# Kernel tuning notes

Hardware: AMD Instinct MI355X
Metric: run time of the kernel (lower is better)

The kernel has to match this reference:

```python
import jax, jax.numpy as jnp
import numpy as np

BETA = 0.95      # LIF leak
LR = 2e-06       # Hebbian learning rate
THRESH = 1.0     # snntorch Leaky default threshold, reset-by-subtraction
NUM_INPUTS = 8192
NUM_HIDDEN = 8192


def surrogate(x):
    # 1 / (pi * (1 + (pi*x)^2))
    return 1.0 / (jnp.pi * (1.0 + (jnp.pi * x) ** 2))


def setup_inputs() -> dict:
    key = jax.random.key(0)
    ks = jax.random.split(key, 8)
    I, H = NUM_INPUTS, NUM_HIDDEN
    inp = jax.random.normal(ks[0], (I,), jnp.float32)
    bf = jnp.float32(1.0)
    fc_w = jax.random.normal(ks[1], (H, I), jnp.float32) / np.float32(np.sqrt(I))
    fc_b = jnp.zeros((H,), jnp.float32)
    pred_w = jax.random.normal(ks[2], (H, H), jnp.float32) / np.float32(np.sqrt(H))
    retro_w = jax.random.normal(ks[3], (H, H), jnp.float32) / np.float32(np.sqrt(H))
    feedback = jax.random.normal(ks[4], (H,), jnp.float32) * 0.1
    mem = jax.random.uniform(ks[5], (H,), jnp.float32)
    cur_prev = jax.random.normal(ks[6], (H,), jnp.float32)
    prev_inp = jax.random.normal(ks[7], (I,), jnp.float32)
    return {"inp": inp, "bf": bf, "fc_w": fc_w, "fc_b": fc_b,
            "pred_w": pred_w, "retro_w": retro_w, "feedback": feedback,
            "mem": mem, "cur_prev": cur_prev, "prev_inp": prev_inp}


def reference(inp, bf, fc_w, fc_b, pred_w, retro_w, feedback, mem, cur_prev, prev_inp):
    # ---- LIF step (snntorch Leaky, reset by subtraction) ----
    cur = fc_w @ inp + fc_b                       # [H]
    mem_new = BETA * mem + cur                    # [H]
    spk = (mem_new > THRESH).astype(cur.dtype)    # [H]
    mem_out = mem_new - spk * THRESH              # [H]

    # ---- Hebbian / CLAPP weight updates (training branch) ----
    retrodiction = retro_w @ spk                  # [H]
    dW_pred = (LR * bf) * jnp.outer(feedback, spk)        # [H,H]
    pred_w_new = pred_w + dW_pred
    retro_w_new = retro_w + dW_pred.T

    # diag(v) @ outer(a, b) == outer(v * a, b): avoid materializing [H,H] diag
    dW = (LR * bf) * jnp.outer(feedback * surrogate(cur), inp)       # [H,I]
    dW = dW + bf * jnp.outer(retrodiction * surrogate(cur_prev), prev_inp)
    fc_w_new = fc_w + dW

    feedback_new = pred_w_new @ spk               # [H]
    return spk, mem_out, fc_w_new, pred_w_new, retro_w_new, feedback_new
```

## Files before the change

kernel.cpp:

```cpp
#include <hip/hip_runtime.h>
#include <math.h>

static constexpr int HN = 8192;
static constexpr int IN = 8192;
static constexpr float LRF = 2.0e-6f;

__device__ __forceinline__ float surrogate_f(float x) {
    const float PI = 3.14159265358979323846f;
    float px = PI * x;
    return 1.0f / (PI * fmaf(px, px, 1.0f));
}

__device__ __forceinline__ float block_reduce_f32(float v) {
#pragma unroll
    for (int off = 32; off > 0; off >>= 1) v += __shfl_down(v, off);
    __shared__ float s[4];
    if ((threadIdx.x & 63) == 0) s[threadIdx.x >> 6] = v;
    __syncthreads();
    return s[0] + s[1] + s[2] + s[3];
}

__global__ __launch_bounds__(256) void k_lif(
    const float* __restrict__ fc_w, const float* __restrict__ inp,
    const float* __restrict__ fc_b, const float* __restrict__ mem,
    float* __restrict__ out_spk, float* __restrict__ out_mem,
    float* __restrict__ ws_cur, float* __restrict__ ws_spk)
{
    const int row = blockIdx.x;
    const int t = threadIdx.x;
    const float4* __restrict__ wr = (const float4*)(fc_w + (size_t)row * IN);
    const float4* __restrict__ ip = (const float4*)inp;
    double acc = 0.0;
#pragma unroll
    for (int j = 0; j < IN / 4 / 256; ++j) {
        float4 w = wr[t + j * 256];
        float4 x = ip[t + j * 256];
        acc += (double)w.x * (double)x.x;
        acc += (double)w.y * (double)x.y;
        acc += (double)w.z * (double)x.z;
        acc += (double)w.w * (double)x.w;
    }
#pragma unroll
    for (int off = 32; off > 0; off >>= 1) acc += __shfl_down(acc, off);
    __shared__ double sacc[4];
    if ((t & 63) == 0) sacc[t >> 6] = acc;
    __syncthreads();
    if (t == 0) {
        double c = sacc[0] + sacc[1] + sacc[2] + sacc[3] + (double)fc_b[row];
        double m = 0.95 * (double)mem[row] + c;
        float spk = (m > 1.0) ? 1.0f : 0.0f;
        out_spk[row] = spk;
        ws_spk[row]  = spk;
        out_mem[row] = (float)(m - (double)spk);
        ws_cur[row]  = (float)c;
    }
}

__global__ __launch_bounds__(256) void k_bc(
    const float* __restrict__ retro_w, const float* __restrict__ pred_w,
    const float* __restrict__ feedback, const float* __restrict__ bfp,
    const float* __restrict__ ws_spk,
    float* __restrict__ out_pred, float* __restrict__ out_retro,
    float* __restrict__ out_fb, float* __restrict__ ws_ret)
{
    const float lrbf = LRF * bfp[0];
    const int t = threadIdx.x;
    const float4* __restrict__ spk4 = (const float4*)ws_spk;
    if (blockIdx.x < HN) {
        const int row = blockIdx.x;
        const float4* __restrict__ wr = (const float4*)(retro_w + (size_t)row * HN);
        float4* __restrict__ orow = (float4*)(out_retro + (size_t)row * HN);
        const float4* __restrict__ fb4 = (const float4*)feedback;
        const float coef = lrbf * ws_spk[row];
        float acc = 0.0f;
#pragma unroll
        for (int j = 0; j < HN / 4 / 256; ++j) {
            int idx = t + j * 256;
            float4 w = wr[idx];
            float4 s = spk4[idx];
            float4 f = fb4[idx];
            acc += w.x * s.x + w.y * s.y + w.z * s.z + w.w * s.w;
            float4 o;
            o.x = w.x + coef * f.x;
            o.y = w.y + coef * f.y;
            o.z = w.z + coef * f.z;
            o.w = w.w + coef * f.w;
            orow[idx] = o;
        }
        float r = block_reduce_f32(acc);
        if (t == 0) ws_ret[row] = r;
    } else {
        const int row = blockIdx.x - HN;
        const float4* __restrict__ wr = (const float4*)(pred_w + (size_t)row * HN);
        float4* __restrict__ orow = (float4*)(out_pred + (size_t)row * HN);
        const float coef = lrbf * feedback[row];
        float acc = 0.0f;
#pragma unroll
        for (int j = 0; j < HN / 4 / 256; ++j) {
            int idx = t + j * 256;
            float4 w = wr[idx];
            float4 s = spk4[idx];
            float4 o;
            o.x = w.x + coef * s.x;
            o.y = w.y + coef * s.y;
            o.z = w.z + coef * s.z;
            o.w = w.w + coef * s.w;
            orow[idx] = o;
            acc += o.x * s.x + o.y * s.y + o.z * s.z + o.w * s.w;
        }
        float r = block_reduce_f32(acc);
        if (t == 0) out_fb[row] = r;
    }
}

__global__ __launch_bounds__(256) void k_fc(
    const float* __restrict__ fc_w, const float* __restrict__ inp,
    const float* __restrict__ prev_inp, const float* __restrict__ feedback,
    const float* __restrict__ cur_prev, const float* __restrict__ bfp,
    const float* __restrict__ ws_cur, const float* __restrict__ ws_ret,
    float* __restrict__ out_fcw)
{
    const float bf = bfp[0];
    const int row = blockIdx.x;
    const int t = threadIdx.x;
    const float a = LRF * bf * feedback[row] * surrogate_f(ws_cur[row]);
    const float b = bf * ws_ret[row] * surrogate_f(cur_prev[row]);
    const float4* __restrict__ wr = (const float4*)(fc_w + (size_t)row * IN);
    const float4* __restrict__ ip = (const float4*)inp;
    const float4* __restrict__ pp = (const float4*)prev_inp;
    float4* __restrict__ orow = (float4*)(out_fcw + (size_t)row * IN);
#pragma unroll
    for (int j = 0; j < IN / 4 / 256; ++j) {
        int idx = t + j * 256;
        float4 w = wr[idx];
        float4 x = ip[idx];
        float4 p = pp[idx];
        float4 o;
        o.x = w.x + a * x.x + b * p.x;
        o.y = w.y + a * x.y + b * p.y;
        o.z = w.z + a * x.z + b * p.z;
        o.w = w.w + a * x.w + b * p.w;
        orow[idx] = o;
    }
}

extern "C" void kernel_launch(void* const* d_in, const int* in_sizes, int n_in,
                              void* d_out, int out_size, void* d_ws, size_t ws_size,
                              hipStream_t stream)
{
    const float* inp      = (const float*)d_in[0];
    const float* bf       = (const float*)d_in[1];
    const float* fc_w     = (const float*)d_in[2];
    const float* fc_b     = (const float*)d_in[3];
    const float* pred_w   = (const float*)d_in[4];
    const float* retro_w  = (const float*)d_in[5];
    const float* feedback = (const float*)d_in[6];
    const float* mem      = (const float*)d_in[7];
    const float* cur_prev = (const float*)d_in[8];
    const float* prev_inp = (const float*)d_in[9];

    float* out = (float*)d_out;
    float* out_spk   = out;
    float* out_mem   = out + HN;
    float* out_fcw   = out + 2 * HN;
    float* out_pred  = out_fcw + (size_t)HN * IN;
    float* out_retro = out_pred + (size_t)HN * HN;
    float* out_fb    = out_retro + (size_t)HN * HN;

    float* ws = (float*)d_ws;
    float* ws_cur = ws;
    float* ws_spk = ws + HN;
    float* ws_ret = ws + 2 * HN;

    k_lif<<<HN, 256, 0, stream>>>(fc_w, inp, fc_b, mem, out_spk, out_mem, ws_cur, ws_spk);
    k_bc<<<2 * HN, 256, 0, stream>>>(retro_w, pred_w, feedback, bf, ws_spk,
                                     out_pred, out_retro, out_fb, ws_ret);
    k_fc<<<HN, 256, 0, stream>>>(fc_w, inp, prev_inp, feedback, cur_prev, bf,
                                 ws_cur, ws_ret, out_fcw);
}
```

Before: 359.1 us.

## Fuse fc_w update into retro block and use nontemporal loads/stores

Merges the fc_w update kernel into the retro_w block, so each retro row computes its retrodiction and then updates the matching fc_w row directly. This drops one launch and the workspace round trip for the retrodiction values. Nontemporal loads and stores are applied to the large weight streams to reduce cache pollution. Block work becomes unbalanced: retro blocks now do two row passes while pred blocks do one, which could lengthen the tail.

```diff
diff --git a/kernel.cpp b/kernel.cpp
--- a/kernel.cpp
+++ b/kernel.cpp
@@ -4,6 +4,8 @@
 static constexpr int HN = 8192;
 static constexpr int IN = 8192;
 static constexpr float LRF = 2.0e-6f;
+
+typedef float f32x4 __attribute__((ext_vector_type(4)));
 
 __device__ __forceinline__ float surrogate_f(float x) {
     const float PI = 3.14159265358979323846f;
@@ -28,13 +30,13 @@
 {
     const int row = blockIdx.x;
     const int t = threadIdx.x;
-    const float4* __restrict__ wr = (const float4*)(fc_w + (size_t)row * IN);
-    const float4* __restrict__ ip = (const float4*)inp;
+    const f32x4* __restrict__ wr = (const f32x4*)(fc_w + (size_t)row * IN);
+    const f32x4* __restrict__ ip = (const f32x4*)inp;
     double acc = 0.0;
 #pragma unroll
     for (int j = 0; j < IN / 4 / 256; ++j) {
-        float4 w = wr[t + j * 256];
-        float4 x = ip[t + j * 256];
+        f32x4 w = wr[t + j * 256];
+        f32x4 x = ip[t + j * 256];
         acc += (double)w.x * (double)x.x;
         acc += (double)w.y * (double)x.y;
         acc += (double)w.z * (double)x.z;
@@ -56,91 +58,83 @@
     }
 }
 
-__global__ __launch_bounds__(256) void k_bc(
+__global__ __launch_bounds__(256) void k_fused(
     const float* __restrict__ retro_w, const float* __restrict__ pred_w,
+    const float* __restrict__ fc_w, const float* __restrict__ inp,
+    const float* __restrict__ prev_inp,
     const float* __restrict__ feedback, const float* __restrict__ bfp,
-    const float* __restrict__ ws_spk,
+    const float* __restrict__ cur_prev,
+    const float* __restrict__ ws_spk, const float* __restrict__ ws_cur,
     float* __restrict__ out_pred, float* __restrict__ out_retro,
-    float* __restrict__ out_fb, float* __restrict__ ws_ret)
+    float* __restrict__ out_fcw, float* __restrict__ out_fb)
 {
-    const float lrbf = LRF * bfp[0];
+    const float bf = bfp[0];
+    const float lrbf = LRF * bf;
     const int t = threadIdx.x;
-    const float4* __restrict__ spk4 = (const float4*)ws_spk;
+    const f32x4* __restrict__ spk4 = (const f32x4*)ws_spk;
+
     if (blockIdx.x < HN) {
         const int row = blockIdx.x;
-        const float4* __restrict__ wr = (const float4*)(retro_w + (size_t)row * HN);
-        float4* __restrict__ orow = (float4*)(out_retro + (size_t)row * HN);
-        const float4* __restrict__ fb4 = (const float4*)feedback;
+        const f32x4* __restrict__ wr = (const f32x4*)(retro_w + (size_t)row * HN);
+        f32x4* __restrict__ orow = (f32x4*)(out_retro + (size_t)row * HN);
+        const f32x4* __restrict__ fb4 = (const f32x4*)feedback;
         const float coef = lrbf * ws_spk[row];
         float acc = 0.0f;
 #pragma unroll
         for (int j = 0; j < HN / 4 / 256; ++j) {
             int idx = t + j * 256;
-            float4 w = wr[idx];
-            float4 s = spk4[idx];
-            float4 f = fb4[idx];
+            f32x4 w = __builtin_nontemporal_load(&wr[idx]);
+            f32x4 s = spk4[idx];
+            f32x4 f = fb4[idx];
             acc += w.x * s.x + w.y * s.y + w.z * s.z + w.w * s.w;
-            float4 o;
+            f32x4 o;
             o.x = w.x + coef * f.x;
             o.y = w.y + coef * f.y;
             o.z = w.z + coef * f.z;
             o.w = w.w + coef * f.w;
-            orow[idx] = o;
+            __builtin_nontemporal_store(o, &orow[idx]);
         }
-        float r = block_reduce_f32(acc);
-        if (t == 0) ws_ret[row] = r;
+        float retrod = block_reduce_f32(acc);
+        const float a = lrbf * feedback[row] * surrogate_f(ws_cur[row]);
+        const float b = bf * retrod * surrogate_f(cur_prev[row]);
+        const f32x4* __restrict__ fwr = (const f32x4*)(fc_w + (size_t)row * IN);
+        const f32x4* __restrict__ ip = (const f32x4*)inp;
+        const f32x4* __restrict__ pp = (const f32x4*)prev_inp;
+        f32x4* __restrict__ forow = (f32x4*)(out_fcw + (size_t)row * IN);
+#pragma unroll
+        for (int j = 0; j < IN / 4 / 256; ++j) {
+            int idx = t + j * 256;
+            f32x4 w = fwr[idx];
+            f32x4 x = ip[idx];
+            f32x4 p = pp[idx];
+            f32x4 o;
+            o.x = w.x + a * x.x + b * p.x;
+            o.y = w.y + a * x.y + b * p.y;
+            o.z = w.z + a * x.z + b * p.z;
+            o.w = w.w + a * x.w + b * p.w;
+            __builtin_nontemporal_store(o, &forow[idx]);
+        }
     } else {
         const int row = blockIdx.x - HN;
-        const float4* __restrict__ wr = (const float4*)(pred_w + (size_t)row * HN);
-        float4* __restrict__ orow = (float4*)(out_pred + (size_t)row * HN);
+        const f32x4* __restrict__ wr = (const f32x4*)(pred_w + (size_t)row * HN);
+        f32x4* __restrict__ orow = (f32x4*)(out_pred + (size_t)row * HN);
         const float coef = lrbf * feedback[row];
         float acc = 0.0f;
 #pragma unroll
         for (int j = 0; j < HN / 4 / 256; ++j) {
             int idx = t + j * 256;
-            float4 w = wr[idx];
-            float4 s = spk4[idx];
-            float4 o;
+            f32x4 w = __builtin_nontemporal_load(&wr[idx]);
+            f32x4 s = spk4[idx];
+            f32x4 o;
             o.x = w.x + coef * s.x;
             o.y = w.y + coef * s.y;
             o.z = w.z + coef * s.z;
             o.w = w.w + coef * s.w;
-            orow[idx] = o;
+            __builtin_nontemporal_store(o, &orow[idx]);
             acc += o.x * s.x + o.y * s.y + o.z * s.z + o.w * s.w;
         }
         float r = block_reduce_f32(acc);
         if (t == 0) out_fb[row] = r;
-    }
-}
-
-__global__ __launch_bounds__(256) void k_fc(
-    const float* __restrict__ fc_w, const float* __restrict__ inp,
-    const float* __restrict__ prev_inp, const float* __restrict__ feedback,
-    const float* __restrict__ cur_prev, const float* __restrict__ bfp,
-    const float* __restrict__ ws_cur, const float* __restrict__ ws_ret,
-    float* __restrict__ out_fcw)
-{
-    const float bf = bfp[0];
-    const int row = blockIdx.x;
-    const int t = threadIdx.x;
-    const float a = LRF * bf * feedback[row] * surrogate_f(ws_cur[row]);
-    const float b = bf * ws_ret[row] * surrogate_f(cur_prev[row]);
-    const float4* __restrict__ wr = (const float4*)(fc_w + (size_t)row * IN);
-    const float4* __restrict__ ip = (const float4*)inp;
-    const float4* __restrict__ pp = (const float4*)prev_inp;
-    float4* __restrict__ orow = (float4*)(out_fcw + (size_t)row * IN);
-#pragma unroll
-    for (int j = 0; j < IN / 4 / 256; ++j) {
-        int idx = t + j * 256;
-        float4 w = wr[idx];
-        float4 x = ip[idx];
-        float4 p = pp[idx];
-        float4 o;
-        o.x = w.x + a * x.x + b * p.x;
-        o.y = w.y + a * x.y + b * p.y;
-        o.z = w.z + a * x.z + b * p.z;
-        o.w = w.w + a * x.w + b * p.w;
-        orow[idx] = o;
     }
 }
 
@@ -170,11 +164,9 @@
     float* ws = (float*)d_ws;
     float* ws_cur = ws;
     float* ws_spk = ws + HN;
-    float* ws_ret = ws + 2 * HN;
 
     k_lif<<<HN, 256, 0, stream>>>(fc_w, inp, fc_b, mem, out_spk, out_mem, ws_cur, ws_spk);
-    k_bc<<<2 * HN, 256, 0, stream>>>(retro_w, pred_w, feedback, bf, ws_spk,
-                                     out_pred, out_retro, out_fb, ws_ret);
-    k_fc<<<HN, 256, 0, stream>>>(fc_w, inp, prev_inp, feedback, cur_prev, bf,
-                                 ws_cur, ws_ret, out_fcw);
+    k_fused<<<2 * HN, 256, 0, stream>>>(retro_w, pred_w, fc_w, inp, prev_inp,
+                                        feedback, bf, cur_prev, ws_spk, ws_cur,
+                                        out_pred, out_retro, out_fcw, out_fb);
 }
```

After: 320.4 us. 1.12x faster.
